# Performance work log

Hardware: AMD Instinct MI355X
Metric: run time of the kernel (lower is better)

## Reference

```python
import jax, jax.numpy as jnp
import numpy as np

ALPHA = 0.1  # cfg.model.mmd.attention_temperature
EPS = 1e-12


def _l2norm(x, axis=-1):
    return x / jnp.sqrt(jnp.sum(x * x, axis=axis, keepdims=True) + EPS)


def setup_inputs() -> dict:
    key = jax.random.key(0)
    k1, k2, k3, k4 = jax.random.split(key, 4)
    b, ng, nl, nf, c = 8, 5, 75, 196, 640
    return {
        "global_f": jax.random.normal(k1, (b, ng, c), dtype=jnp.float32),
        "local_f": jax.random.normal(k2, (b, nl, nf, c), dtype=jnp.float32),
        "Wq": jax.random.normal(k3, (c, c), dtype=jnp.float32) / np.sqrt(c),
        "Wk": jax.random.normal(k4, (c, c), dtype=jnp.float32) / np.sqrt(c),
    }


def reference(global_f, local_f, Wq, Wk):
    # AttentiveMMDPrompt.compute_attn_weight with dim=1, num_groups=1.
    b, ng, c = global_f.shape
    _, nl, nf, _ = local_f.shape
    # q/k projections (nn.Linear, no bias): x @ W^T
    g = jnp.einsum('bgc,dc->bgd', global_f, Wq)          # [b, ng, c]
    l = jnp.einsum('blfc,dc->blfd', local_f, Wk)         # [b, nl, nf, c]
    # centering: subtract joint per-episode mean feature over all tokens
    tot = g.sum(axis=1) + l.sum(axis=(1, 2))             # [b, c]
    mean = tot / (ng + nl * nf)
    g = g - mean[:, None, :]
    l = l - mean[:, None, None, :]
    # l2 normalize feature vectors
    g = _l2norm(g)
    l = _l2norm(l)
    # score: local_f @ global_f -> [b, nl, ng, nf]
    scores = jnp.einsum('blfc,bgc->blgf', l, g) / ALPHA
    attn = jax.nn.softmax(scores, axis=-1)               # softmax over nf
    return attn[..., None]                               # [b, nl, ng, nf, 1]
```

## Files before the change

kernel.cpp:

```cpp
#include <hip/hip_runtime.h>
#include <math.h>

namespace {
constexpr int kB = 8, kNG = 5, kNL = 75, kNF = 196, kC = 640;
constexpr int kNTokL = kNL * kNF;
constexpr int kNTot = kNG + kNTokL;
constexpr float kEps = 1e-12f;
constexpr float kInvAlpha = 10.0f;
constexpr int kKC = 20;
constexpr int kTiles = 230;
constexpr int kNT = 5;
}

typedef __attribute__((ext_vector_type(8))) short short8;
typedef __attribute__((ext_vector_type(4))) short short4v;
typedef __attribute__((ext_vector_type(4))) float floatx4;

union S8U { short8 v; ushort u[8]; };
union S4U { short4v v; ushort u[4]; };

__device__ __forceinline__ void bsplit(float x, ushort& h, ushort& l) {
  union { float f; uint u; } a; a.f = x;
  uint uh = (a.u + 0x7FFFu + ((a.u >> 16) & 1u)) >> 16;
  h = (ushort)uh;
  union { uint u; float f; } bb; bb.u = uh << 16;
  float r = x - bb.f;
  union { float f; uint u; } c; c.f = r;
  l = (ushort)((c.u + 0x7FFFu + ((c.u >> 16) & 1u)) >> 16);
}

#define MFMA_BF16(a, b, c) __builtin_amdgcn_mfma_f32_16x16x32_bf16(a, b, c, 0, 0, 0)

__device__ __forceinline__ void bar_lds() {
  asm volatile("s_waitcnt lgkmcnt(0)\n\ts_barrier" ::: "memory");
}


__global__ void k_sum_local(const float* __restrict__ lf, float* __restrict__ s_l) {
  const int b = blockIdx.x, slice = blockIdx.y;
  const int tid = threadIdx.x;
  const int c4 = tid % 160, h = tid / 160;
  const int t0 = slice * 115 + h * 58;
  const int nrow = min(h ? 57 : 58, kNTokL - t0);
  const float* p = lf + ((size_t)b * kNTokL + t0) * kC + c4 * 4;
  float4 acc = {0.f, 0.f, 0.f, 0.f};
#pragma unroll 2
  for (int i = 0; i < nrow; ++i) {
    const float4 v = *(const float4*)(p + (size_t)i * kC);
    acc.x += v.x; acc.y += v.y; acc.z += v.z; acc.w += v.w;
  }
  float* dst = &s_l[b * kC + c4 * 4];
  atomicAdd(dst + 0, acc.x);
  atomicAdd(dst + 1, acc.y);
  atomicAdd(dst + 2, acc.z);
  atomicAdd(dst + 3, acc.w);
}

__global__ void k_cvtW(const float* __restrict__ Wk, ushort* __restrict__ Wh,
                       ushort* __restrict__ Wl) {
  const int wv = blockIdx.x * 4 + (threadIdx.x >> 6);
  const int lane = threadIdx.x & 63;
  const int kc = wv % kKC, dt = wv / kKC;
  const int fm = lane & 15, quad = lane >> 4;
  const float* p = Wk + (size_t)(dt * 16 + fm) * kC + kc * 32 + quad * 8;
  float4 a = *(const float4*)p;
  float4 c = *(const float4*)(p + 4);
  S8U h, l;
  bsplit(a.x, h.u[0], l.u[0]); bsplit(a.y, h.u[1], l.u[1]);
  bsplit(a.z, h.u[2], l.u[2]); bsplit(a.w, h.u[3], l.u[3]);
  bsplit(c.x, h.u[4], l.u[4]); bsplit(c.y, h.u[5], l.u[5]);
  bsplit(c.z, h.u[6], l.u[6]); bsplit(c.w, h.u[7], l.u[7]);
  const size_t off = ((size_t)kc * 40 + dt) * 512 + (size_t)lane * 8;
  *(short8*)(Wh + off) = h.v;
  *(short8*)(Wl + off) = l.v;
}

__global__ void k_proj_mean(const float* __restrict__ Wq, const float* __restrict__ Wk,
                            const float* __restrict__ gf, const float* __restrict__ s_l,
                            float* __restrict__ m, float* __restrict__ gc) {
  const int wid = blockIdx.x * 4 + (threadIdx.x >> 6);
  const int lane = threadIdx.x & 63;
  const int b = wid / kC, d = wid % kC;
  float ak = 0.f, ag[kNG] = {0.f, 0.f, 0.f, 0.f, 0.f};
  for (int c = lane; c < kC; c += 64) {
    const float wq = Wq[d * kC + c];
    const float wk = Wk[d * kC + c];
    ak += wk * s_l[b * kC + c];
#pragma unroll
    for (int g = 0; g < kNG; ++g) ag[g] += wq * gf[(b * kNG + g) * kC + c];
  }
#pragma unroll
  for (int off = 32; off > 0; off >>= 1) {
    ak += __shfl_xor(ak, off);
#pragma unroll
    for (int g = 0; g < kNG; ++g) ag[g] += __shfl_xor(ag[g], off);
  }
  if (lane == 0) {
    float aq = 0.f;
#pragma unroll
    for (int g = 0; g < kNG; ++g) aq += ag[g];
    const float mv = (aq + ak) / (float)kNTot;
    m[b * kC + d] = mv;
#pragma unroll
    for (int g = 0; g < kNG; ++g) gc[(b * kNG + g) * kC + d] = ag[g] - mv;
  }
}

__global__ void k_norm_g(const float* __restrict__ gc, float* __restrict__ gn) {
  const int row = blockIdx.x;
  __shared__ float red[256];
  float a = 0.f;
  for (int d = threadIdx.x; d < kC; d += 256) {
    const float v = gc[row * kC + d];
    a += v * v;
  }
  red[threadIdx.x] = a;
  __syncthreads();
  for (int s = 128; s > 0; s >>= 1) {
    if (threadIdx.x < s) red[threadIdx.x] += red[threadIdx.x + s];
    __syncthreads();
  }
  const float rs = 1.0f / sqrtf(red[0] + kEps);
  for (int d = threadIdx.x; d < kC; d += 256) gn[row * kC + d] = gc[row * kC + d] * rs;
}

__global__ __launch_bounds__(512, 1) void k_big(
    const float* __restrict__ lf, const ushort* __restrict__ Wh,
    const ushort* __restrict__ Wl, const float* __restrict__ m,
    const float* __restrict__ gn, float* __restrict__ scores) {
  __shared__ char smem[32768];
  ushort* A0 = (ushort*)smem;
  ushort* A1 = (ushort*)(smem + 16384);
  float* red = (float*)smem;

  const int tid = threadIdx.x;
  const int wn = tid >> 6, lane = tid & 63;
  const int fm = lane & 15, quad = lane >> 4;
  const int b = blockIdx.x & 7, tile = blockIdx.x >> 3;
  const int tok0 = tile * 64;

  const int sr = tid >> 3, sq = tid & 7;
  const int st = tok0 + sr;
  const bool sok = st < kNTokL;
  const float* xrow = lf + ((size_t)b * kNTokL + st) * kC + sq * 4;
  const int aoff = ((sr >> 4) << 9) + (((sq >> 1) * 16 + (sr & 15)) << 3) + ((sq & 1) << 2);

  floatx4 acc[4][kNT];
#pragma unroll
  for (int i = 0; i < 4; ++i)
#pragma unroll
    for (int j = 0; j < kNT; ++j) acc[i][j] = (floatx4){0.f, 0.f, 0.f, 0.f};

#define STAGE_A(XV, AB, CI)                                   \
  {                                                           \
    S4U _h, _l;                                               \
    bsplit((XV).x, _h.u[0], _l.u[0]);                         \
    bsplit((XV).y, _h.u[1], _l.u[1]);                         \
    bsplit((XV).z, _h.u[2], _l.u[2]);                         \
    bsplit((XV).w, _h.u[3], _l.u[3]);                         \
    *(short4v*)((AB) + (CI) * 2048 + aoff) = _h.v;            \
    *(short4v*)((AB) + 4096 + (CI) * 2048 + aoff) = _l.v;     \
  }

#define LOADB(BH, BL, KCI)                                                        \
  {                                                                               \
    const size_t _o = ((size_t)(KCI) * 40 + wn * 5) * 512 + (size_t)lane * 8;     \
    _Pragma("unroll") for (int nt = 0; nt < kNT; ++nt) {                          \
      BH[nt] = *(const short8*)(Wh + _o + nt * 512);                              \
      BL[nt] = *(const short8*)(Wl + _o + nt * 512);                              \
    }                                                                             \
  }

#define READA(AB, CI)                                                             \
  {                                                                               \
    _Pragma("unroll") for (int mt = 0; mt < 4; ++mt) {                            \
      ah[mt] = *(const short8*)((AB) + (CI) * 2048 + mt * 512 + lane * 8);        \
      al[mt] = *(const short8*)((AB) + 4096 + (CI) * 2048 + mt * 512 + lane * 8); \
    }                                                                             \
  }

#define DOMFMA3(BH, BL)                                                \
  {                                                                    \
    _Pragma("unroll") for (int nt = 0; nt < kNT; ++nt)                 \
        _Pragma("unroll") for (int mt = 0; mt < 4; ++mt)               \
            acc[mt][nt] = MFMA_BF16(ah[mt], BH[nt], acc[mt][nt]);      \
    _Pragma("unroll") for (int nt = 0; nt < kNT; ++nt)                 \
        _Pragma("unroll") for (int mt = 0; mt < 4; ++mt)               \
            acc[mt][nt] = MFMA_BF16(al[mt], BH[nt], acc[mt][nt]);      \
    _Pragma("unroll") for (int nt = 0; nt < kNT; ++nt)                 \
        _Pragma("unroll") for (int mt = 0; mt < 4; ++mt)               \
            acc[mt][nt] = MFMA_BF16(ah[mt], BL[nt], acc[mt][nt]);      \
  }

  const float4 fzero = {0.f, 0.f, 0.f, 0.f};
  float4 x0 = sok ? *(const float4*)xrow : fzero;
  float4 x1 = sok ? *(const float4*)(xrow + 32) : fzero;
  STAGE_A(x0, A0, 0);
  STAGE_A(x1, A0, 1);
  float4 xA0 = sok ? *(const float4*)(xrow + 64) : fzero;
  float4 xA1 = sok ? *(const float4*)(xrow + 96) : fzero;
  float4 xB0 = fzero, xB1 = fzero;
  short8 BH0[kNT], BL0[kNT], BH1[kNT], BL1[kNT];
  LOADB(BH0, BL0, 0);

  short8 ah[4], al[4];
  ushort* Ac = A0;
  ushort* An = A1;
  for (int kc = 0; kc < kKC; kc += 2) {
    bar_lds();
    READA(Ac, 0);
    LOADB(BH1, BL1, kc + 1);
    if (sok && kc + 4 < kKC) {
      xB0 = *(const float4*)(xrow + (kc + 4) * 32);
      xB1 = *(const float4*)(xrow + (kc + 5) * 32);
    }
    if (kc + 2 < kKC) {
      STAGE_A(xA0, An, 0);
      STAGE_A(xA1, An, 1);
    }
    DOMFMA3(BH0, BL0);
    READA(Ac, 1);
    if (kc + 2 < kKC) LOADB(BH0, BL0, kc + 2);
    xA0 = xB0; xA1 = xB1;
    DOMFMA3(BH1, BL1);
    ushort* tswap = Ac; Ac = An; An = tswap;
  }

  float mv[kNT], gvv[5][kNT];
#pragma unroll
  for (int nt = 0; nt < kNT; ++nt) {
    const int d = wn * 80 + nt * 16 + fm;
    mv[nt] = m[b * kC + d];
#pragma unroll
    for (int g = 0; g < 5; ++g) gvv[g][nt] = gn[(b * kNG + g) * kC + d];
  }

  bar_lds();
#pragma unroll
  for (int mt = 0; mt < 4; ++mt)
#pragma unroll
    for (int reg = 0; reg < 4; ++reg) {
      float part[6] = {0.f, 0.f, 0.f, 0.f, 0.f, 0.f};
#pragma unroll
      for (int nt = 0; nt < kNT; ++nt) {
        const float yc = acc[mt][nt][reg] - mv[nt];
        part[0] += yc * yc;
#pragma unroll
        for (int g = 0; g < 5; ++g) part[1 + g] += yc * gvv[g][nt];
      }
#pragma unroll
      for (int off = 1; off < 16; off <<= 1)
#pragma unroll
        for (int v = 0; v < 6; ++v) part[v] += __shfl_xor(part[v], off);
      if (fm == 0) {
        const int row = mt * 16 + quad * 4 + reg;
#pragma unroll
        for (int v = 0; v < 6; ++v) red[((size_t)wn * 64 + row) * 6 + v] = part[v];
      }
    }
  bar_lds();
  if (tid < 64) {
    const int tok = tok0 + tid;
    if (tok < kNTokL) {
      float s[6] = {0.f, 0.f, 0.f, 0.f, 0.f, 0.f};
#pragma unroll
      for (int w = 0; w < 8; ++w)
#pragma unroll
        for (int v = 0; v < 6; ++v) s[v] += red[((size_t)w * 64 + tid) * 6 + v];
      const float rs = (1.0f / sqrtf(s[0] + kEps)) * kInvAlpha;
      const size_t t = (size_t)b * kNTokL + tok;
#pragma unroll
      for (int g = 0; g < 5; ++g)
        scores[(size_t)g * (kB * kNTokL) + t] = s[1 + g] * rs;
    }
  }
#undef STAGE_A
#undef LOADB
#undef READA
#undef DOMFMA3
}

__global__ void k_softmax(const float* __restrict__ scores, float* __restrict__ out) {
  const int wid = blockIdx.x * 4 + (threadIdx.x >> 6);
  const int lane = threadIdx.x & 63;
  const int b = wid / (kNL * kNG);
  const int rem = wid % (kNL * kNG);
  const int l = rem / kNG, g = rem % kNG;
  float sv[4];
  float mx = -1e30f;
#pragma unroll
  for (int u = 0; u < 4; ++u) {
    const int f = lane + 64 * u;
    if (f < kNF) {
      const size_t t = (size_t)b * kNTokL + (size_t)l * kNF + f;
      sv[u] = scores[(size_t)g * (kB * kNTokL) + t];
      mx = fmaxf(mx, sv[u]);
    } else {
      sv[u] = 0.f;
    }
  }
#pragma unroll
  for (int off = 32; off > 0; off >>= 1) mx = fmaxf(mx, __shfl_xor(mx, off));
  float se = 0.f;
#pragma unroll
  for (int u = 0; u < 4; ++u) {
    const int f = lane + 64 * u;
    const float e = (f < kNF) ? expf(sv[u] - mx) : 0.f;
    sv[u] = e;
    se += e;
  }
#pragma unroll
  for (int off = 32; off > 0; off >>= 1) se += __shfl_xor(se, off);
  const float inv = 1.0f / se;
#pragma unroll
  for (int u = 0; u < 4; ++u) {
    const int f = lane + 64 * u;
    if (f < kNF) out[((size_t)(b * kNL + l) * kNG + g) * kNF + f] = sv[u] * inv;
  }
}


extern "C" void kernel_launch(void* const* d_in, const int* in_sizes, int n_in,
                              void* d_out, int out_size, void* d_ws, size_t ws_size,
                              hipStream_t stream) {
  (void)in_sizes; (void)n_in; (void)out_size; (void)ws_size;
  const float* gf = (const float*)d_in[0];
  const float* lf = (const float*)d_in[1];
  const float* Wq = (const float*)d_in[2];
  const float* Wk = (const float*)d_in[3];
  float* ws = (float*)d_ws;
  float* out = (float*)d_out;

  float* s_l    = ws;
  float* m      = ws + 5120;
  float* gc     = ws + 10240;
  float* gn     = ws + 35840;
  float* scores = ws + 61440;
  ushort* Wh    = (ushort*)(ws + 649440);
  ushort* Wl    = (ushort*)(ws + 854240);

  hipMemsetAsync(s_l, 0, (size_t)5120 * 4, stream);

  k_sum_local<<<dim3(kB, 128), 320, 0, stream>>>(lf, s_l);
  k_cvtW<<<200, 256, 0, stream>>>(Wk, Wh, Wl);
  k_proj_mean<<<(kB * kC) / 4, 256, 0, stream>>>(Wq, Wk, gf, s_l, m, gc);
  k_norm_g<<<kB * kNG, 256, 0, stream>>>(gc, gn);
  k_big<<<kTiles * kB, 512, 0, stream>>>(lf, Wh, Wl, m, gn, scores);
  k_softmax<<<750, 256, 0, stream>>>(scores, out);
}
```

Before: 811.2 us.

## Stream A tiles via global_load_lds and split to bf16 after LDS read

The main projection kernel now copies fp32 local features straight into LDS with global_load_lds in 128-wide K chunks, double-buffered. The hi/lo bf16 split moves to after the LDS read, and the B fragments are loaded from global one N-tile ahead instead of in large register batches. This is meant to take the register round-trip out of the A staging and ease register pressure, at the cost of twice the LDS footprint and redundant bsplit work. Separately, the local-sum kernel reduces its two halves in shared memory before issuing atomics and launches half as many blocks.

```diff
diff --git a/kernel.cpp b/kernel.cpp
--- a/kernel.cpp
+++ b/kernel.cpp
@@ -13,11 +13,9 @@
 }
 
 typedef __attribute__((ext_vector_type(8))) short short8;
-typedef __attribute__((ext_vector_type(4))) short short4v;
 typedef __attribute__((ext_vector_type(4))) float floatx4;
 
 union S8U { short8 v; ushort u[8]; };
-union S4U { short4v v; ushort u[4]; };
 
 __device__ __forceinline__ void bsplit(float x, ushort& h, ushort& l) {
   union { float f; uint u; } a; a.f = x;
@@ -35,13 +33,19 @@
   asm volatile("s_waitcnt lgkmcnt(0)\n\ts_barrier" ::: "memory");
 }
 
+__device__ __forceinline__ void gld_lds16(const float* g, float* l) {
+  __builtin_amdgcn_global_load_lds(
+      (const __attribute__((address_space(1))) void*)g,
+      (__attribute__((address_space(3))) void*)l, 16, 0, 0);
+}
+
 
 __global__ void k_sum_local(const float* __restrict__ lf, float* __restrict__ s_l) {
   const int b = blockIdx.x, slice = blockIdx.y;
   const int tid = threadIdx.x;
   const int c4 = tid % 160, h = tid / 160;
-  const int t0 = slice * 115 + h * 58;
-  const int nrow = min(h ? 57 : 58, kNTokL - t0);
+  const int t0 = slice * 230 + h * 115;
+  const int nrow = min(115, kNTokL - t0);
   const float* p = lf + ((size_t)b * kNTokL + t0) * kC + c4 * 4;
   float4 acc = {0.f, 0.f, 0.f, 0.f};
 #pragma unroll 2
@@ -49,11 +53,18 @@
     const float4 v = *(const float4*)(p + (size_t)i * kC);
     acc.x += v.x; acc.y += v.y; acc.z += v.z; acc.w += v.w;
   }
-  float* dst = &s_l[b * kC + c4 * 4];
-  atomicAdd(dst + 0, acc.x);
-  atomicAdd(dst + 1, acc.y);
-  atomicAdd(dst + 2, acc.z);
-  atomicAdd(dst + 3, acc.w);
+  __shared__ float4 sred[160];
+  if (h == 1) sred[c4] = acc;
+  __syncthreads();
+  if (h == 0) {
+    const float4 o = sred[c4];
+    acc.x += o.x; acc.y += o.y; acc.z += o.z; acc.w += o.w;
+    float* dst = &s_l[b * kC + c4 * 4];
+    atomicAdd(dst + 0, acc.x);
+    atomicAdd(dst + 1, acc.y);
+    atomicAdd(dst + 2, acc.z);
+    atomicAdd(dst + 3, acc.w);
+  }
 }
 
 __global__ void k_cvtW(const float* __restrict__ Wk, ushort* __restrict__ Wh,
@@ -128,10 +139,8 @@
     const float* __restrict__ lf, const ushort* __restrict__ Wh,
     const ushort* __restrict__ Wl, const float* __restrict__ m,
     const float* __restrict__ gn, float* __restrict__ scores) {
-  __shared__ char smem[32768];
-  ushort* A0 = (ushort*)smem;
-  ushort* A1 = (ushort*)(smem + 16384);
-  float* red = (float*)smem;
+  __shared__ float smem[16384];
+  float* red = smem;
 
   const int tid = threadIdx.x;
   const int wn = tid >> 6, lane = tid & 63;
@@ -139,11 +148,13 @@
   const int b = blockIdx.x & 7, tile = blockIdx.x >> 3;
   const int tok0 = tile * 64;
 
-  const int sr = tid >> 3, sq = tid & 7;
-  const int st = tok0 + sr;
-  const bool sok = st < kNTokL;
-  const float* xrow = lf + ((size_t)b * kNTokL + st) * kC + sq * 4;
-  const int aoff = ((sr >> 4) << 9) + (((sq >> 1) * 16 + (sr & 15)) << 3) + ((sq & 1) << 2);
+  const int ti0 = wn * 2;
+  int r0 = tok0 + (ti0 & 3) * 16 + fm;
+  int r1 = tok0 + ((ti0 + 1) & 3) * 16 + fm;
+  if (r0 >= kNTokL) r0 = kNTokL - 1;
+  if (r1 >= kNTokL) r1 = kNTokL - 1;
+  const float* sg0 = lf + ((size_t)b * kNTokL + r0) * kC + (ti0 >> 2) * 32 + quad * 8;
+  const float* sg1 = lf + ((size_t)b * kNTokL + r1) * kC + ((ti0 + 1) >> 2) * 32 + quad * 8;
 
   floatx4 acc[4][kNT];
 #pragma unroll
@@ -151,79 +162,65 @@
 #pragma unroll
     for (int j = 0; j < kNT; ++j) acc[i][j] = (floatx4){0.f, 0.f, 0.f, 0.f};
 
-#define STAGE_A(XV, AB, CI)                                   \
-  {                                                           \
-    S4U _h, _l;                                               \
-    bsplit((XV).x, _h.u[0], _l.u[0]);                         \
-    bsplit((XV).y, _h.u[1], _l.u[1]);                         \
-    bsplit((XV).z, _h.u[2], _l.u[2]);                         \
-    bsplit((XV).w, _h.u[3], _l.u[3]);                         \
-    *(short4v*)((AB) + (CI) * 2048 + aoff) = _h.v;            \
-    *(short4v*)((AB) + 4096 + (CI) * 2048 + aoff) = _l.v;     \
-  }
-
-#define LOADB(BH, BL, KCI)                                                        \
-  {                                                                               \
-    const size_t _o = ((size_t)(KCI) * 40 + wn * 5) * 512 + (size_t)lane * 8;     \
-    _Pragma("unroll") for (int nt = 0; nt < kNT; ++nt) {                          \
-      BH[nt] = *(const short8*)(Wh + _o + nt * 512);                              \
-      BL[nt] = *(const short8*)(Wl + _o + nt * 512);                              \
-    }                                                                             \
-  }
-
-#define READA(AB, CI)                                                             \
-  {                                                                               \
-    _Pragma("unroll") for (int mt = 0; mt < 4; ++mt) {                            \
-      ah[mt] = *(const short8*)((AB) + (CI) * 2048 + mt * 512 + lane * 8);        \
-      al[mt] = *(const short8*)((AB) + 4096 + (CI) * 2048 + mt * 512 + lane * 8); \
-    }                                                                             \
-  }
-
-#define DOMFMA3(BH, BL)                                                \
-  {                                                                    \
-    _Pragma("unroll") for (int nt = 0; nt < kNT; ++nt)                 \
-        _Pragma("unroll") for (int mt = 0; mt < 4; ++mt)               \
-            acc[mt][nt] = MFMA_BF16(ah[mt], BH[nt], acc[mt][nt]);      \
-    _Pragma("unroll") for (int nt = 0; nt < kNT; ++nt)                 \
-        _Pragma("unroll") for (int mt = 0; mt < 4; ++mt)               \
-            acc[mt][nt] = MFMA_BF16(al[mt], BH[nt], acc[mt][nt]);      \
-    _Pragma("unroll") for (int nt = 0; nt < kNT; ++nt)                 \
-        _Pragma("unroll") for (int mt = 0; mt < 4; ++mt)               \
-            acc[mt][nt] = MFMA_BF16(ah[mt], BL[nt], acc[mt][nt]);      \
-  }
-
-  const float4 fzero = {0.f, 0.f, 0.f, 0.f};
-  float4 x0 = sok ? *(const float4*)xrow : fzero;
-  float4 x1 = sok ? *(const float4*)(xrow + 32) : fzero;
-  STAGE_A(x0, A0, 0);
-  STAGE_A(x1, A0, 1);
-  float4 xA0 = sok ? *(const float4*)(xrow + 64) : fzero;
-  float4 xA1 = sok ? *(const float4*)(xrow + 96) : fzero;
-  float4 xB0 = fzero, xB1 = fzero;
-  short8 BH0[kNT], BL0[kNT], BH1[kNT], BL1[kNT];
-  LOADB(BH0, BL0, 0);
+#define ISSUE_A(BUFF, KC128)                                        \
+  {                                                                 \
+    const float* _s0 = sg0 + (KC128) * 128;                         \
+    const float* _s1 = sg1 + (KC128) * 128;                         \
+    float* _d = smem + (BUFF) + ti0 * 512;                          \
+    gld_lds16(_s0, _d);                                             \
+    gld_lds16(_s0 + 4, _d + 256);                                   \
+    gld_lds16(_s1, _d + 512);                                       \
+    gld_lds16(_s1 + 4, _d + 768);                                   \
+  }
+
+#define READCVT(BUFF, S)                                                      \
+  {                                                                           \
+    _Pragma("unroll") for (int mt = 0; mt < 4; ++mt) {                        \
+      const float* _t = smem + (BUFF) + ((S) * 4 + mt) * 512;                 \
+      floatx4 f0 = *(const floatx4*)(_t + lane * 4);                          \
+      floatx4 f1 = *(const floatx4*)(_t + 256 + lane * 4);                    \
+      S8U _h, _l;                                                             \
+      bsplit(f0[0], _h.u[0], _l.u[0]); bsplit(f0[1], _h.u[1], _l.u[1]);       \
+      bsplit(f0[2], _h.u[2], _l.u[2]); bsplit(f0[3], _h.u[3], _l.u[3]);       \
+      bsplit(f1[0], _h.u[4], _l.u[4]); bsplit(f1[1], _h.u[5], _l.u[5]);       \
+      bsplit(f1[2], _h.u[6], _l.u[6]); bsplit(f1[3], _h.u[7], _l.u[7]);       \
+      ah[mt] = _h.v; al[mt] = _l.v;                                           \
+    }                                                                         \
+  }
+
+#define DOSUB(BUFF, S, KCI)                                                   \
+  {                                                                           \
+    READCVT(BUFF, S);                                                         \
+    const ushort* _bh = Wh + ((size_t)(KCI) * 40 + wn * 5) * 512 + (size_t)lane * 8; \
+    const ushort* _bl = Wl + ((size_t)(KCI) * 40 + wn * 5) * 512 + (size_t)lane * 8; \
+    short8 bhc = *(const short8*)_bh;                                         \
+    short8 blc = *(const short8*)_bl;                                         \
+    _Pragma("unroll") for (int nt = 0; nt < kNT; ++nt) {                      \
+      short8 bhn = bhc, bln = blc;                                            \
+      if (nt + 1 < kNT) {                                                     \
+        bhn = *(const short8*)(_bh + (nt + 1) * 512);                         \
+        bln = *(const short8*)(_bl + (nt + 1) * 512);                         \
+      }                                                                       \
+      _Pragma("unroll") for (int mt = 0; mt < 4; ++mt)                        \
+          acc[mt][nt] = MFMA_BF16(ah[mt], bhc, acc[mt][nt]);                  \
+      _Pragma("unroll") for (int mt = 0; mt < 4; ++mt)                        \
+          acc[mt][nt] = MFMA_BF16(al[mt], bhc, acc[mt][nt]);                  \
+      _Pragma("unroll") for (int mt = 0; mt < 4; ++mt)                        \
+          acc[mt][nt] = MFMA_BF16(ah[mt], blc, acc[mt][nt]);                  \
+      bhc = bhn; blc = bln;                                                   \
+    }                                                                         \
+  }
 
   short8 ah[4], al[4];
-  ushort* Ac = A0;
-  ushort* An = A1;
-  for (int kc = 0; kc < kKC; kc += 2) {
-    bar_lds();
-    READA(Ac, 0);
-    LOADB(BH1, BL1, kc + 1);
-    if (sok && kc + 4 < kKC) {
-      xB0 = *(const float4*)(xrow + (kc + 4) * 32);
-      xB1 = *(const float4*)(xrow + (kc + 5) * 32);
-    }
-    if (kc + 2 < kKC) {
-      STAGE_A(xA0, An, 0);
-      STAGE_A(xA1, An, 1);
-    }
-    DOMFMA3(BH0, BL0);
-    READA(Ac, 1);
-    if (kc + 2 < kKC) LOADB(BH0, BL0, kc + 2);
-    xA0 = xB0; xA1 = xB1;
-    DOMFMA3(BH1, BL1);
-    ushort* tswap = Ac; Ac = An; An = tswap;
+  ISSUE_A(0, 0);
+  for (int t = 0; t < 5; ++t) {
+    const int buff = (t & 1) * 8192;
+    asm volatile("s_waitcnt vmcnt(0) lgkmcnt(0)\n\ts_barrier" ::: "memory");
+    if (t < 4) ISSUE_A(((t & 1) ^ 1) * 8192, t + 1);
+    DOSUB(buff, 0, t * 4 + 0);
+    DOSUB(buff, 1, t * 4 + 1);
+    DOSUB(buff, 2, t * 4 + 2);
+    DOSUB(buff, 3, t * 4 + 3);
   }
 
   float mv[kNT], gvv[5][kNT];
@@ -274,10 +271,9 @@
         scores[(size_t)g * (kB * kNTokL) + t] = s[1 + g] * rs;
     }
   }
-#undef STAGE_A
-#undef LOADB
-#undef READA
-#undef DOMFMA3
+#undef ISSUE_A
+#undef READCVT
+#undef DOSUB
 }
 
 __global__ void k_softmax(const float* __restrict__ scores, float* __restrict__ out) {
@@ -341,7 +337,7 @@
 
   hipMemsetAsync(s_l, 0, (size_t)5120 * 4, stream);
 
-  k_sum_local<<<dim3(kB, 128), 320, 0, stream>>>(lf, s_l);
+  k_sum_local<<<dim3(kB, 64), 320, 0, stream>>>(lf, s_l);
   k_cvtW<<<200, 256, 0, stream>>>(Wk, Wh, Wl);
   k_proj_mean<<<(kB * kC) / 4, 256, 0, stream>>>(Wq, Wk, gf, s_l, m, gc);
   k_norm_g<<<kB * kNG, 256, 0, stream>>>(gc, gn);
```

After: 1.047 ms. +29.1%, slower.
